# Optimization experiments

Hardware: AMD Instinct MI355X
Metric: run time of the kernel (lower is better)

## Reference

```python
import jax, jax.numpy as jnp
import numpy as np

B, N, D, H = 2, 2048, 512, 8
DH = D  # head_subspaces=False -> d_head = d_model
F = H * DH  # 4096, projected feature dim (RoPE applied over this full dim)


def rotate_half(x):
    # interleaved pairs (lucidrains rotary-embedding-torch default): (x0,x1)->(-x1,x0)
    x2 = x.reshape(*x.shape[:-1], -1, 2)
    return jnp.stack([-x2[..., 1], x2[..., 0]], axis=-1).reshape(x.shape)


def apply_rope(x, cos, sin):
    # x: [B,N,F], cos/sin: [N,F]
    return x * cos[None] + rotate_half(x) * sin[None]


def setup_inputs() -> dict:
    key = jax.random.key(0)
    kx, kq, kk, kv, ko = jax.random.split(key, 5)
    x = jax.random.normal(kx, (B, N, D), dtype=jnp.float32)
    # rotary tables over full projected dim, freqs repeated in interleaved pairs
    inv_freq = 1.0 / (10000.0 ** (jnp.arange(0, F, 2, dtype=jnp.float32) / F))
    freqs = jnp.arange(N, dtype=jnp.float32)[:, None] * inv_freq[None, :]  # [N, F/2]
    freqs = jnp.repeat(freqs, 2, axis=-1)  # [N, F], pairwise interleaved
    cos, sin = jnp.cos(freqs), jnp.sin(freqs)
    # causal bool mask [B, query, target] (3-dim branch of the module)
    target_mask = jnp.broadcast_to(jnp.tril(jnp.ones((N, N), dtype=bool))[None], (B, N, N))
    s = 0.02
    Wq = jax.random.normal(kq, (D, F), dtype=jnp.float32) * s
    Wk = jax.random.normal(kk, (D, F), dtype=jnp.float32) * s
    Wv = jax.random.normal(kv, (D, F), dtype=jnp.float32) * s
    bv = jnp.zeros((F,), dtype=jnp.float32)
    Wo = jax.random.normal(ko, (D, D), dtype=jnp.float32) * s
    bo = jnp.zeros((D,), dtype=jnp.float32)
    return {"x": x, "cos": cos, "sin": sin, "target_mask": target_mask,
            "Wq": Wq, "Wk": Wk, "Wv": Wv, "bv": bv, "Wo": Wo, "bo": bo}


def reference(x, cos, sin, target_mask, Wq, Wk, Wv, bv, Wo, bo):
    b, n, d = x.shape
    Q = apply_rope(x @ Wq, cos, sin)  # RoPE on full [B,N,F] projection
    K = apply_rope(x @ Wk, cos, sin)
    V = x @ Wv + bv
    # split heads: [B,H,N,DH]
    Q = Q.reshape(b, n, H, DH).transpose(0, 2, 1, 3)
    K = K.reshape(b, n, H, DH).transpose(0, 2, 1, 3)
    V = V.reshape(b, n, H, DH).transpose(0, 2, 1, 3)
    A = jnp.einsum('bhid,bhjd->bhij', Q, K)  # NOTE: no 1/sqrt(d) scaling, as in source
    A = jnp.where(target_mask[:, None, :, :], A, -jnp.inf)
    A = jax.nn.softmax(A, axis=-1)
    y = jnp.einsum('bhij,bhjd->bhid', A, V)
    # head_subspaces=False: merge heads by SUM over head axis -> [B,N,D]
    y = y.sum(axis=1)
    y = y * jax.nn.sigmoid(1.702 * y)  # QuickGELU
    return y @ Wo + bo
```

## Files before the change

### kernel.cpp

```cpp
#include <hip/hip_runtime.h>

typedef unsigned short u16;
typedef u16 u16x8 __attribute__((ext_vector_type(8)));
typedef __bf16 bf16x8 __attribute__((ext_vector_type(8)));
typedef float f32x4 __attribute__((ext_vector_type(4)));

#define DEV __device__ __forceinline__
#define MFMA16 __builtin_amdgcn_mfma_f32_16x16x32_bf16

constexpr int Bb = 2, Nctx = 2048, Dm = 512, Hh = 8, Dh = 512, Ff = 4096;
constexpr int Mrows = Bb * Nctx;

DEV float b2f(u16 u) { unsigned int i = ((unsigned int)u) << 16; return __builtin_bit_cast(float, i); }
DEV u16 f2b(float f) {
  unsigned int x = __builtin_bit_cast(unsigned int, f);
  return (u16)((x + 0x7FFFu + ((x >> 16) & 1u)) >> 16);
}
DEV bf16x8 ld8(const u16* p) { return __builtin_bit_cast(bf16x8, *(const u16x8*)p); }

DEV void gload16(const u16* g, u16* l) {
#if defined(__has_builtin) && __has_builtin(__builtin_amdgcn_global_load_lds)
  __builtin_amdgcn_global_load_lds((const __attribute__((address_space(1))) void*)(g),
                                   (__attribute__((address_space(3))) void*)(l), 16, 0, 0);
#else
  *(u16x8*)l = *(const u16x8*)g;
#endif
}

__global__ void convert_k(const float* __restrict__ in, u16* __restrict__ out, int n8) {
  int idx = blockIdx.x * 256 + threadIdx.x;
  if (idx >= n8) return;
  size_t e0 = (size_t)idx * 8;
  f32x4 a = *(const f32x4*)(in + e0);
  f32x4 b = *(const f32x4*)(in + e0 + 4);
  u16x8 o;
  #pragma unroll
  for (int i = 0; i < 4; ++i) { o[i] = f2b(a[i]); o[4 + i] = f2b(b[i]); }
  *(u16x8*)(out + e0) = o;
}

__global__ void transpose_k(const float* __restrict__ in, u16* __restrict__ out,
                            int rows, int cols) {
  __shared__ float tile[32][33];
  int bx = blockIdx.x * 32, by = blockIdx.y * 32;
  int tx = threadIdx.x, ty = threadIdx.y;
  #pragma unroll
  for (int i = ty; i < 32; i += 8)
    tile[i][tx] = in[(size_t)(by + i) * cols + bx + tx];
  __syncthreads();
  #pragma unroll
  for (int i = ty; i < 32; i += 8)
    out[(size_t)(bx + i) * rows + by + tx] = f2b(tile[tx][i]);
}

__global__ void vtrans_k(const u16* __restrict__ V, u16* __restrict__ Vt) {
  __shared__ u16 tile[64 * 64];
  const int z = blockIdx.z;
  const int b = z >> 3, h = z & 7;
  const int n0 = blockIdx.x * 64, d0 = blockIdx.y * 64;
  const int t = threadIdx.x;
  const int nl = t >> 3;
  const int dg = t & 7;
  #pragma unroll
  for (int sw = 0; sw < 2; ++sw) {
    int n = nl + 32 * sw;
    u16x8 v = *(const u16x8*)&V[((size_t)(b * Nctx + n0 + n)) * Ff + h * Dh + d0 + dg * 8];
    #pragma unroll
    for (int j = 0; j < 8; ++j) {
      int d = dg * 8 + j;
      int g = ((d & 7) ^ (d >> 3)) & 7;
      tile[d * 64 + (n ^ (g << 3))] = v[j];
    }
  }
  __syncthreads();
  #pragma unroll
  for (int sw = 0; sw < 2; ++sw) {
    int d = nl + 32 * sw;
    int g = ((d & 7) ^ (d >> 3)) & 7;
    u16x8 v = *(const u16x8*)&tile[d * 64 + ((dg ^ g) << 3)];
    *(u16x8*)&Vt[((size_t)(z * Dh + d0 + d)) * Nctx + n0 + dg * 8] = v;
  }
}

template <int MODE>
__launch_bounds__(256, 4)
__global__ void gemm2_k(const u16* __restrict__ A, const u16* __restrict__ BT,
                        void* __restrict__ Cout, const float* __restrict__ bias,
                        const float* __restrict__ cs, const float* __restrict__ sn,
                        int Ndim, int Kdim) {
  __shared__ u16 sA[128 * 64];
  __shared__ u16 sB[128 * 64];
  const int tid = threadIdx.x;
  const int wave = tid >> 6, lane = tid & 63, quad = lane >> 4, l16 = lane & 15;
  const int wy = wave >> 1, wx = wave & 1;
  const int m0 = blockIdx.y * 128, n0 = blockIdx.x * 128;
  f32x4 acc[4][4];
  #pragma unroll
  for (int i = 0; i < 4; ++i)
    #pragma unroll
    for (int j = 0; j < 4; ++j)
      #pragma unroll
      for (int r = 0; r < 4; ++r) acc[i][j][r] = 0.f;
  const int srow = tid >> 3;
  const int scol = (tid & 7) * 8;
  for (int k0 = 0; k0 < Kdim; k0 += 64) {
    __syncthreads();
    #pragma unroll
    for (int sw = 0; sw < 4; ++sw) {
      int row = srow + 32 * sw;
      int sc = scol ^ ((row & 7) * 8);
      gload16(A + (size_t)(m0 + row) * Kdim + k0 + sc, &sA[row * 64 + scol]);
      gload16(BT + (size_t)(n0 + row) * Kdim + k0 + sc, &sB[row * 64 + scol]);
    }
    __syncthreads();
    #pragma unroll
    for (int kk2 = 0; kk2 < 2; ++kk2) {
      const int cbase = (kk2 * 32 + quad * 8) ^ ((l16 & 7) * 8);
      bf16x8 af[4], bf[4];
      #pragma unroll
      for (int t = 0; t < 4; ++t) af[t] = ld8(&sA[(wy * 64 + t * 16 + l16) * 64 + cbase]);
      #pragma unroll
      for (int t = 0; t < 4; ++t) bf[t] = ld8(&sB[(wx * 64 + t * 16 + l16) * 64 + cbase]);
      #pragma unroll
      for (int i = 0; i < 4; ++i)
        #pragma unroll
        for (int j = 0; j < 4; ++j)
          acc[i][j] = MFMA16(af[i], bf[j], acc[i][j], 0, 0, 0);
    }
  }
  #pragma unroll
  for (int i = 0; i < 4; ++i) {
    #pragma unroll
    for (int j = 0; j < 4; ++j) {
      int col = n0 + wx * 64 + j * 16 + l16;
      float badd = (MODE == 2 || MODE == 3) ? bias[col] : 0.f;
      #pragma unroll
      for (int r = 0; r < 4; ++r) {
        int row = m0 + wy * 64 + i * 16 + quad * 4 + r;
        float v = acc[i][j][r] + badd;
        if (MODE == 1) {
          float vp = __shfl_xor(v, 1);
          int n = row & (Nctx - 1);
          float c = cs[(size_t)n * Ff + col];
          float s = sn[(size_t)n * Ff + col];
          v = (l16 & 1) ? (v * c + vp * s) : (v * c - vp * s);
        }
        if (MODE == 3) ((float*)Cout)[(size_t)row * Ndim + col] = v;
        else           ((u16*)Cout)[(size_t)row * Ndim + col] = f2b(v);
      }
    }
  }
}

__launch_bounds__(256, 1)
__global__ void attn_k(const u16* __restrict__ Q, const u16* __restrict__ K,
                       const u16* __restrict__ Vt, u16* __restrict__ Yp) {
  __shared__ u16 sK[64 * 512];
  __shared__ u16 sP[64 * 72];
  __shared__ float sAl[64];
  __shared__ float sL[64];
  const int idx = blockIdx.x;
  const int hi = idx >> 8;
  const int bh = (idx & 7) | (hi << 3);
  const int q_ = (idx >> 3) & 31;
  const int zig = (q_ & 1) ? (31 - (q_ >> 1)) : (q_ >> 1);
  const int qt = hi ? (31 - zig) : zig;
  const int b = bh >> 3, h = bh & 7;
  const int q0 = qt * 64;
  const int wave = threadIdx.x >> 6, lane = threadIdx.x & 63;
  const int quad = lane >> 4, l16 = lane & 15;
  const int mq = q0 + wave * 16;
  const int wd = wave * 128;

  bf16x8 qf[16];
  {
    const u16* qp = Q + ((size_t)(b * Nctx + mq + l16)) * Ff + h * Dh + quad * 8;
    #pragma unroll
    for (int i = 0; i < 16; ++i) qf[i] = ld8(qp + i * 32);
  }
  f32x4 acc[4][8];
  #pragma unroll
  for (int g = 0; g < 4; ++g)
    #pragma unroll
    for (int t = 0; t < 8; ++t)
      #pragma unroll
      for (int r = 0; r < 4; ++r) acc[g][t][r] = 0.f;
  float mrun[4], lrun[4];
  #pragma unroll
  for (int r = 0; r < 4; ++r) { mrun[r] = -__builtin_inff(); lrun[r] = 0.f; }

  auto stageK = [&](int j0) {
    #pragma unroll
    for (int it = 0; it < 16; ++it) {
      int row = wave * 16 + it;
      const u16* gp = K + ((size_t)(b * Nctx + j0 + row)) * Ff + h * Dh + (((lane - row) & 63) * 8);
      gload16(gp, &sK[row * 512 + lane * 8]);
    }
  };
  const u16* vrow = Vt + ((size_t)(bh * Dh + wd + l16)) * Nctx;

  stageK(0);
  for (int jt = 0; jt <= qt; ++jt) {
    const int j0 = jt * 64;
    __syncthreads();
    f32x4 s[4];
    #pragma unroll
    for (int kg = 0; kg < 4; ++kg)
      #pragma unroll
      for (int r = 0; r < 4; ++r) s[kg][r] = 0.f;
    #pragma unroll
    for (int kk = 0; kk < 16; ++kk) {
      #pragma unroll
      for (int kg = 0; kg < 4; ++kg) {
        int key = kg * 16 + l16;
        bf16x8 bfr = ld8(&sK[key * 512 + (((kk * 4 + quad + key) & 63) * 8)]);
        s[kg] = MFMA16(qf[kk], bfr, s[kg], 0, 0, 0);
      }
    }
    const bool diag = (jt == qt);
    float p[4][4], alpha[4];
    #pragma unroll
    for (int r = 0; r < 4; ++r) {
      int qrow = mq + quad * 4 + r;
      float sv[4];
      #pragma unroll
      for (int kg = 0; kg < 4; ++kg) {
        int key = j0 + kg * 16 + l16;
        sv[kg] = (diag && key > qrow) ? -__builtin_inff() : s[kg][r];
      }
      float mx = fmaxf(fmaxf(sv[0], sv[1]), fmaxf(sv[2], sv[3]));
      mx = fmaxf(mx, __shfl_xor(mx, 1));
      mx = fmaxf(mx, __shfl_xor(mx, 2));
      mx = fmaxf(mx, __shfl_xor(mx, 4));
      mx = fmaxf(mx, __shfl_xor(mx, 8));
      float mnew = fmaxf(mrun[r], mx);
      float a = __expf(mrun[r] - mnew);
      float rs = 0.f;
      #pragma unroll
      for (int kg = 0; kg < 4; ++kg) { float pe = __expf(sv[kg] - mnew); p[r][kg] = pe; rs += pe; }
      lrun[r] = lrun[r] * a + rs;
      mrun[r] = mnew;
      alpha[r] = a;
    }
    #pragma unroll
    for (int r = 0; r < 4; ++r) {
      #pragma unroll
      for (int kg = 0; kg < 4; ++kg)
        sP[(wave * 16 + quad * 4 + r) * 72 + kg * 16 + l16] = f2b(p[r][kg]);
      if (l16 == 0) sAl[wave * 16 + quad * 4 + r] = alpha[r];
    }
    __syncthreads();
    if (jt < qt) stageK(j0 + 64);
    {
      #pragma unroll
      for (int g = 0; g < 4; ++g) {
        float a0 = sAl[g * 16 + quad * 4 + 0];
        float a1 = sAl[g * 16 + quad * 4 + 1];
        float a2 = sAl[g * 16 + quad * 4 + 2];
        float a3 = sAl[g * 16 + quad * 4 + 3];
        #pragma unroll
        for (int t = 0; t < 8; ++t) {
          acc[g][t][0] *= a0; acc[g][t][1] *= a1; acc[g][t][2] *= a2; acc[g][t][3] *= a3;
        }
      }
      bf16x8 pf[4][2];
      #pragma unroll
      for (int g = 0; g < 4; ++g)
        #pragma unroll
        for (int kk = 0; kk < 2; ++kk)
          pf[g][kk] = ld8(&sP[(g * 16 + l16) * 72 + kk * 32 + quad * 8]);
      #pragma unroll
      for (int t = 0; t < 8; ++t) {
        const u16* vp = vrow + (size_t)(t * 16) * Nctx + j0 + quad * 8;
        bf16x8 v0 = ld8(vp);
        bf16x8 v1 = ld8(vp + 32);
        #pragma unroll
        for (int g = 0; g < 4; ++g) acc[g][t] = MFMA16(pf[g][0], v0, acc[g][t], 0, 0, 0);
        #pragma unroll
        for (int g = 0; g < 4; ++g) acc[g][t] = MFMA16(pf[g][1], v1, acc[g][t], 0, 0, 0);
      }
    }
  }
  #pragma unroll
  for (int r = 0; r < 4; ++r) {
    float l = lrun[r];
    l += __shfl_xor(l, 1);
    l += __shfl_xor(l, 2);
    l += __shfl_xor(l, 4);
    l += __shfl_xor(l, 8);
    if (l16 == 0) sL[wave * 16 + quad * 4 + r] = l;
  }
  __syncthreads();
  #pragma unroll
  for (int g = 0; g < 4; ++g) {
    float inv[4];
    #pragma unroll
    for (int r = 0; r < 4; ++r) inv[r] = 1.f / sL[g * 16 + quad * 4 + r];
    #pragma unroll
    for (int t = 0; t < 8; ++t)
      #pragma unroll
      for (int r = 0; r < 4; ++r)
        Yp[((size_t)bh * Nctx + q0 + g * 16 + quad * 4 + r) * Dh + wd + t * 16 + l16] =
            f2b(acc[g][t][r] * inv[r]);
  }
}

__global__ void sumheads_k(const u16* __restrict__ Yp, u16* __restrict__ Ys) {
  size_t idx = (size_t)blockIdx.x * 256 + threadIdx.x;
  size_t e0 = idx * 8;
  int b = (int)(e0 >> 20);
  size_t rem = e0 & ((1u << 20) - 1);
  float s[8];
  #pragma unroll
  for (int e = 0; e < 8; ++e) s[e] = 0.f;
  #pragma unroll
  for (int h = 0; h < Hh; ++h) {
    u16x8 v = *(const u16x8*)&Yp[((size_t)(b * Hh + h) << 20) + rem];
    #pragma unroll
    for (int e = 0; e < 8; ++e) s[e] += b2f(v[e]);
  }
  u16x8 o;
  #pragma unroll
  for (int e = 0; e < 8; ++e) {
    float g = s[e] / (1.f + __expf(-1.702f * s[e]));
    o[e] = f2b(g);
  }
  *(u16x8*)&Ys[e0] = o;
}

extern "C" void kernel_launch(void* const* d_in, const int* in_sizes, int n_in,
                              void* d_out, int out_size, void* d_ws, size_t ws_size,
                              hipStream_t stream) {
  const float* x  = (const float*)d_in[0];
  const float* cs = (const float*)d_in[1];
  const float* sn = (const float*)d_in[2];
  int wbase = 4;
  if (n_in == 9) wbase = 3;
  if (wbase + 3 < n_in && in_sizes[wbase + 3] != 4096) wbase = (wbase == 4) ? 3 : 4;
  const float* Wq = (const float*)d_in[wbase + 0];
  const float* Wk = (const float*)d_in[wbase + 1];
  const float* Wv = (const float*)d_in[wbase + 2];
  const float* bv = (const float*)d_in[wbase + 3];
  const float* Wo = (const float*)d_in[wbase + 4];
  const float* bo = (const float*)d_in[wbase + 5];

  char* ws = (char*)d_ws;
  const size_t MiB = 1ull << 20;
  u16* WqT = (u16*)(ws + 0 * MiB);
  u16* WkT = (u16*)(ws + 4 * MiB);
  u16* WvT = (u16*)(ws + 8 * MiB);
  u16* xb  = (u16*)(ws + 12 * MiB);
  u16* Vt  = (u16*)(ws + 0 * MiB);
  u16* Qb  = (u16*)(ws + 32 * MiB);
  u16* Kb  = (u16*)(ws + 64 * MiB);
  u16* Vb  = (u16*)(ws + 96 * MiB);
  u16* Yp  = Vb;
  u16* WoT = (u16*)(ws + 128 * MiB);
  u16* Ys  = (u16*)(ws + 128 * MiB + 512 * 1024);

  dim3 tb(32, 8);
  transpose_k<<<dim3(Ff / 32, Dm / 32), tb, 0, stream>>>(Wq, WqT, Dm, Ff);
  transpose_k<<<dim3(Ff / 32, Dm / 32), tb, 0, stream>>>(Wk, WkT, Dm, Ff);
  transpose_k<<<dim3(Ff / 32, Dm / 32), tb, 0, stream>>>(Wv, WvT, Dm, Ff);
  transpose_k<<<dim3(Dm / 32, Dm / 32), tb, 0, stream>>>(Wo, WoT, Dm, Dm);
  convert_k<<<dim3(Mrows * Dm / 8 / 256), 256, 0, stream>>>(x, xb, Mrows * Dm / 8);

  gemm2_k<1><<<dim3(Ff / 128, Mrows / 128), 256, 0, stream>>>(xb, WqT, Qb, nullptr, cs, sn, Ff, Dm);
  gemm2_k<1><<<dim3(Ff / 128, Mrows / 128), 256, 0, stream>>>(xb, WkT, Kb, nullptr, cs, sn, Ff, Dm);
  gemm2_k<2><<<dim3(Ff / 128, Mrows / 128), 256, 0, stream>>>(xb, WvT, Vb, bv, nullptr, nullptr, Ff, Dm);

  vtrans_k<<<dim3(Nctx / 64, Dh / 64, Bb * Hh), 256, 0, stream>>>(Vb, Vt);

  attn_k<<<dim3(512), 256, 0, stream>>>(Qb, Kb, Vt, Yp);

  sumheads_k<<<dim3(Mrows * Dm / 8 / 256), 256, 0, stream>>>(Yp, Ys);

  gemm2_k<3><<<dim3(Dm / 128, Mrows / 128), 256, 0, stream>>>(Ys, WoT, d_out, bo, nullptr, nullptr, Dm, Dm);
}
```

Baseline: 556.8 us.

## Warp-specialize attention into QK/softmax and PV wave groups with pipelined tiles

Rewrites the attention kernel to run 512 threads where four waves compute QK^T scores and softmax while the other four waves stage K and accumulate P·V for the previous tile, using double-buffered P and alpha in shared memory. Query tiles shrink from 64 to 32 rows, and each block processes a pair of tiles (p and 63-p) so the causal work is balanced per block. Q fragments are now reloaded from global memory on every tile instead of being held in registers. The aim is to overlap the score/softmax stage with the PV MFMA stage and reduce register pressure, at the cost of extra barriers and repeated Q loads.

```diff
diff --git a/kernel.cpp b/kernel.cpp
--- a/kernel.cpp
+++ b/kernel.cpp
@@ -152,156 +152,177 @@
   }
 }
 
-__launch_bounds__(256, 1)
+__launch_bounds__(512, 1)
 __global__ void attn_k(const u16* __restrict__ Q, const u16* __restrict__ K,
                        const u16* __restrict__ Vt, u16* __restrict__ Yp) {
-  __shared__ u16 sK[64 * 512];
-  __shared__ u16 sP[64 * 72];
-  __shared__ float sAl[64];
-  __shared__ float sL[64];
+  __shared__ u16 sK[32 * 512];
+  __shared__ float sS[32 * 36];
+  __shared__ u16 sP[2][32 * 40];
+  __shared__ float sAl[2][32];
+  __shared__ float sL[32];
   const int idx = blockIdx.x;
-  const int hi = idx >> 8;
+  const int hi = (idx >> 8) & 1;
   const int bh = (idx & 7) | (hi << 3);
-  const int q_ = (idx >> 3) & 31;
-  const int zig = (q_ & 1) ? (31 - (q_ >> 1)) : (q_ >> 1);
-  const int qt = hi ? (31 - zig) : zig;
+  const int p = (idx >> 3) & 31;
   const int b = bh >> 3, h = bh & 7;
-  const int q0 = qt * 64;
   const int wave = threadIdx.x >> 6, lane = threadIdx.x & 63;
   const int quad = lane >> 4, l16 = lane & 15;
-  const int mq = q0 + wave * 16;
-  const int wd = wave * 128;
-
-  bf16x8 qf[16];
-  {
-    const u16* qp = Q + ((size_t)(b * Nctx + mq + l16)) * Ff + h * Dh + quad * 8;
-    #pragma unroll
-    for (int i = 0; i < 16; ++i) qf[i] = ld8(qp + i * 32);
-  }
-  f32x4 acc[4][8];
-  #pragma unroll
-  for (int g = 0; g < 4; ++g)
-    #pragma unroll
-    for (int t = 0; t < 8; ++t)
-      #pragma unroll
-      for (int r = 0; r < 4; ++r) acc[g][t][r] = 0.f;
-  float mrun[4], lrun[4];
-  #pragma unroll
-  for (int r = 0; r < 4; ++r) { mrun[r] = -__builtin_inff(); lrun[r] = 0.f; }
+  const bool isA = (wave < 4);
+  const int rowg = (wave >> 1) & 1;
+  const int keyg = wave & 1;
+  const int wb = wave & 3;
+  const int wd = wb * 128;
 
   auto stageK = [&](int j0) {
     #pragma unroll
-    for (int it = 0; it < 16; ++it) {
-      int row = wave * 16 + it;
+    for (int it = 0; it < 8; ++it) {
+      int row = wb * 8 + it;
       const u16* gp = K + ((size_t)(b * Nctx + j0 + row)) * Ff + h * Dh + (((lane - row) & 63) * 8);
       gload16(gp, &sK[row * 512 + lane * 8]);
     }
   };
   const u16* vrow = Vt + ((size_t)(bh * Dh + wd + l16)) * Nctx;
 
-  stageK(0);
-  for (int jt = 0; jt <= qt; ++jt) {
-    const int j0 = jt * 64;
+  for (int phase = 0; phase < 2; ++phase) {
+    const int qt = phase ? (63 - p) : p;
+    const bool asc = (phase == 0);
+    const int q0 = qt * 32;
+    const int NT = qt + 1;
+
+    f32x4 acc[2][8];
+    float mrun[4], lrun[4];
+    const u16* qp = Q + ((size_t)(b * Nctx + q0 + rowg * 16 + l16)) * Ff + h * Dh + quad * 8;
+    if (isA) {
+      #pragma unroll
+      for (int r = 0; r < 4; ++r) { mrun[r] = -__builtin_inff(); lrun[r] = 0.f; }
+    } else {
+      #pragma unroll
+      for (int g = 0; g < 2; ++g)
+        #pragma unroll
+        for (int t = 0; t < 8; ++t)
+          #pragma unroll
+          for (int r = 0; r < 4; ++r) acc[g][t][r] = 0.f;
+      stageK((asc ? 0 : qt) * 32);
+    }
     __syncthreads();
-    f32x4 s[4];
-    #pragma unroll
-    for (int kg = 0; kg < 4; ++kg)
-      #pragma unroll
-      for (int r = 0; r < 4; ++r) s[kg][r] = 0.f;
-    #pragma unroll
-    for (int kk = 0; kk < 16; ++kk) {
-      #pragma unroll
-      for (int kg = 0; kg < 4; ++kg) {
-        int key = kg * 16 + l16;
-        bf16x8 bfr = ld8(&sK[key * 512 + (((kk * 4 + quad + key) & 63) * 8)]);
-        s[kg] = MFMA16(qf[kk], bfr, s[kg], 0, 0, 0);
-      }
-    }
-    const bool diag = (jt == qt);
-    float p[4][4], alpha[4];
-    #pragma unroll
-    for (int r = 0; r < 4; ++r) {
-      int qrow = mq + quad * 4 + r;
-      float sv[4];
-      #pragma unroll
-      for (int kg = 0; kg < 4; ++kg) {
-        int key = j0 + kg * 16 + l16;
-        sv[kg] = (diag && key > qrow) ? -__builtin_inff() : s[kg][r];
-      }
-      float mx = fmaxf(fmaxf(sv[0], sv[1]), fmaxf(sv[2], sv[3]));
-      mx = fmaxf(mx, __shfl_xor(mx, 1));
-      mx = fmaxf(mx, __shfl_xor(mx, 2));
-      mx = fmaxf(mx, __shfl_xor(mx, 4));
-      mx = fmaxf(mx, __shfl_xor(mx, 8));
-      float mnew = fmaxf(mrun[r], mx);
-      float a = __expf(mrun[r] - mnew);
-      float rs = 0.f;
-      #pragma unroll
-      for (int kg = 0; kg < 4; ++kg) { float pe = __expf(sv[kg] - mnew); p[r][kg] = pe; rs += pe; }
-      lrun[r] = lrun[r] * a + rs;
-      mrun[r] = mnew;
-      alpha[r] = a;
-    }
-    #pragma unroll
-    for (int r = 0; r < 4; ++r) {
-      #pragma unroll
-      for (int kg = 0; kg < 4; ++kg)
-        sP[(wave * 16 + quad * 4 + r) * 72 + kg * 16 + l16] = f2b(p[r][kg]);
-      if (l16 == 0) sAl[wave * 16 + quad * 4 + r] = alpha[r];
-    }
-    __syncthreads();
-    if (jt < qt) stageK(j0 + 64);
-    {
-      #pragma unroll
-      for (int g = 0; g < 4; ++g) {
-        float a0 = sAl[g * 16 + quad * 4 + 0];
-        float a1 = sAl[g * 16 + quad * 4 + 1];
-        float a2 = sAl[g * 16 + quad * 4 + 2];
-        float a3 = sAl[g * 16 + quad * 4 + 3];
-        #pragma unroll
-        for (int t = 0; t < 8; ++t) {
-          acc[g][t][0] *= a0; acc[g][t][1] *= a1; acc[g][t][2] *= a2; acc[g][t][3] *= a3;
+
+    for (int s = 0; s <= NT; ++s) {
+      if (s > 0) __syncthreads();
+      const int jts = asc ? s : (qt - s);
+      const int jtp = asc ? (s - 1) : (qt - s + 1);
+      if (isA) {
+        if (s < NT) {
+          f32x4 sqk;
+          #pragma unroll
+          for (int r = 0; r < 4; ++r) sqk[r] = 0.f;
+          const int key = keyg * 16 + l16;
+          #pragma unroll 4
+          for (int kk = 0; kk < 16; ++kk) {
+            bf16x8 qfr = ld8(qp + kk * 32);
+            bf16x8 kfr = ld8(&sK[key * 512 + (((kk * 4 + quad + key) & 63) * 8)]);
+            sqk = MFMA16(qfr, kfr, sqk, 0, 0, 0);
+          }
+          #pragma unroll
+          for (int r = 0; r < 4; ++r)
+            sS[(rowg * 16 + quad * 4 + r) * 36 + keyg * 16 + l16] = sqk[r];
+        } else if (wave < 2) {
+          #pragma unroll
+          for (int r = 0; r < 4; ++r) {
+            float l = lrun[r];
+            l += __shfl_xor(l, 1);
+            l += __shfl_xor(l, 2);
+            l += __shfl_xor(l, 4);
+            l += __shfl_xor(l, 8);
+            if (l16 == 0) sL[wave * 16 + quad * 4 + r] = l;
+          }
+        }
+      } else {
+        if (s >= 1) {
+          const int pp = (s - 1) & 1;
+          const int j0p = jtp * 32;
+          float alr[2][4];
+          #pragma unroll
+          for (int g = 0; g < 2; ++g)
+            #pragma unroll
+            for (int r = 0; r < 4; ++r) alr[g][r] = sAl[pp][g * 16 + quad * 4 + r];
+          #pragma unroll
+          for (int g = 0; g < 2; ++g)
+            #pragma unroll
+            for (int t = 0; t < 8; ++t) {
+              acc[g][t][0] *= alr[g][0]; acc[g][t][1] *= alr[g][1];
+              acc[g][t][2] *= alr[g][2]; acc[g][t][3] *= alr[g][3];
+            }
+          bf16x8 pf[2];
+          #pragma unroll
+          for (int g = 0; g < 2; ++g)
+            pf[g] = ld8(&sP[pp][(g * 16 + l16) * 40 + quad * 8]);
+          #pragma unroll
+          for (int t = 0; t < 8; ++t) {
+            bf16x8 v = ld8(vrow + (size_t)(t * 16) * Nctx + j0p + quad * 8);
+            #pragma unroll
+            for (int g = 0; g < 2; ++g)
+              acc[g][t] = MFMA16(pf[g], v, acc[g][t], 0, 0, 0);
+          }
         }
       }
-      bf16x8 pf[4][2];
-      #pragma unroll
-      for (int g = 0; g < 4; ++g)
+      asm volatile("s_waitcnt lgkmcnt(0)" ::: "memory");
+      __builtin_amdgcn_s_barrier();
+      __builtin_amdgcn_sched_barrier(0);
+      if (isA) {
+        if (s < NT && wave < 2) {
+          const bool diag = (jts == qt);
+          const int j0 = jts * 32;
+          const int pg = s & 1;
+          #pragma unroll
+          for (int r = 0; r < 4; ++r) {
+            const int lrow = wave * 16 + quad * 4 + r;
+            const int qrow = q0 + lrow;
+            float sv[2];
+            #pragma unroll
+            for (int kg = 0; kg < 2; ++kg) {
+              int keyj = j0 + kg * 16 + l16;
+              float x = sS[lrow * 36 + kg * 16 + l16];
+              sv[kg] = (diag && keyj > qrow) ? -__builtin_inff() : x;
+            }
+            float mx = fmaxf(sv[0], sv[1]);
+            mx = fmaxf(mx, __shfl_xor(mx, 1));
+            mx = fmaxf(mx, __shfl_xor(mx, 2));
+            mx = fmaxf(mx, __shfl_xor(mx, 4));
+            mx = fmaxf(mx, __shfl_xor(mx, 8));
+            float mnew = fmaxf(mrun[r], mx);
+            float a = __expf(mrun[r] - mnew);
+            float rs = 0.f;
+            #pragma unroll
+            for (int kg = 0; kg < 2; ++kg) {
+              float pe = __expf(sv[kg] - mnew);
+              sP[pg][lrow * 40 + kg * 16 + l16] = f2b(pe);
+              rs += pe;
+            }
+            lrun[r] = lrun[r] * a + rs;
+            mrun[r] = mnew;
+            if (l16 == 0) sAl[pg][lrow] = a;
+          }
+        }
+      } else {
+        if (s + 1 < NT) stageK((asc ? (s + 1) : (qt - s - 1)) * 32);
+      }
+    }
+    __syncthreads();
+    if (!isA) {
+      #pragma unroll
+      for (int g = 0; g < 2; ++g) {
+        float inv[4];
         #pragma unroll
-        for (int kk = 0; kk < 2; ++kk)
-          pf[g][kk] = ld8(&sP[(g * 16 + l16) * 72 + kk * 32 + quad * 8]);
-      #pragma unroll
-      for (int t = 0; t < 8; ++t) {
-        const u16* vp = vrow + (size_t)(t * 16) * Nctx + j0 + quad * 8;
-        bf16x8 v0 = ld8(vp);
-        bf16x8 v1 = ld8(vp + 32);
+        for (int r = 0; r < 4; ++r) inv[r] = 1.f / sL[g * 16 + quad * 4 + r];
         #pragma unroll
-        for (int g = 0; g < 4; ++g) acc[g][t] = MFMA16(pf[g][0], v0, acc[g][t], 0, 0, 0);
-        #pragma unroll
-        for (int g = 0; g < 4; ++g) acc[g][t] = MFMA16(pf[g][1], v1, acc[g][t], 0, 0, 0);
+        for (int t = 0; t < 8; ++t)
+          #pragma unroll
+          for (int r = 0; r < 4; ++r)
+            Yp[((size_t)bh * Nctx + q0 + g * 16 + quad * 4 + r) * Dh + wd + t * 16 + l16] =
+                f2b(acc[g][t][r] * inv[r]);
       }
     }
-  }
-  #pragma unroll
-  for (int r = 0; r < 4; ++r) {
-    float l = lrun[r];
-    l += __shfl_xor(l, 1);
-    l += __shfl_xor(l, 2);
-    l += __shfl_xor(l, 4);
-    l += __shfl_xor(l, 8);
-    if (l16 == 0) sL[wave * 16 + quad * 4 + r] = l;
-  }
-  __syncthreads();
-  #pragma unroll
-  for (int g = 0; g < 4; ++g) {
-    float inv[4];
-    #pragma unroll
-    for (int r = 0; r < 4; ++r) inv[r] = 1.f / sL[g * 16 + quad * 4 + r];
-    #pragma unroll
-    for (int t = 0; t < 8; ++t)
-      #pragma unroll
-      for (int r = 0; r < 4; ++r)
-        Yp[((size_t)bh * Nctx + q0 + g * 16 + quad * 4 + r) * Dh + wd + t * 16 + l16] =
-            f2b(acc[g][t][r] * inv[r]);
+    if (phase == 0) __syncthreads();
   }
 }
 
@@ -371,7 +392,7 @@
 
   vtrans_k<<<dim3(Nctx / 64, Dh / 64, Bb * Hh), 256, 0, stream>>>(Vb, Vt);
 
-  attn_k<<<dim3(512), 256, 0, stream>>>(Qb, Kb, Vt, Yp);
+  attn_k<<<dim3(512), 512, 0, stream>>>(Qb, Kb, Vt, Yp);
 
   sumheads_k<<<dim3(Mrows * Dm / 8 / 256), 256, 0, stream>>>(Yp, Ys);
 
```

New measurement: 846.0 us. 51.9% more time.
